# Performance work log

Measured on AMD Instinct MI355X. Metric: run time of the kernel, lower is better.

Reference implementation:

```python
import jax, jax.numpy as jnp
import numpy as np

NUM_SEG = 16384   # number of ranking lists (scope entries)
SEG_LEN = 512     # items per list
N = NUM_SEG * SEG_LEN


def setup_inputs() -> dict:
    key = jax.random.key(0)
    k1, k2, k3 = jax.random.split(key, 3)
    mean = jax.random.normal(k1, (N, 1), dtype=jnp.float32)
    variance = jax.random.uniform(k2, (N, 1), dtype=jnp.float32)
    targets = jax.random.normal(k3, (N,), dtype=jnp.float32)
    scope = jnp.full((NUM_SEG,), SEG_LEN, dtype=jnp.int32)  # segment lengths
    return {"mean": mean, "variance": variance, "scope": scope, "targets": targets}


def _seg_logsumexp(a, seg, num_segments):
    # numerically-stable segment-wise logsumexp (same math as log(sum(exp)))
    m = jax.ops.segment_max(a, seg, num_segments=num_segments)
    m = jnp.where(jnp.isfinite(m), m, jnp.zeros_like(m))
    s = jax.ops.segment_sum(jnp.exp(a - m[seg]), seg, num_segments=num_segments)
    return m + jnp.log(s)


def reference(mean, variance, scope, targets):
    num_segments = scope.shape[0]
    n = mean.shape[0]
    seg = jnp.repeat(jnp.arange(num_segments), scope, total_repeat_length=n)

    x = mean[:, 0]
    y = variance[:, 0]

    # Original per-segment math: pred_i = 1 / sum_j exp(x_j - x_i + (y_i + y_j)/2)
    #                           = exp(x_i - y_i/2) / sum_j exp(x_j + y_j/2)
    a = x + 0.5 * y
    logS = _seg_logsumexp(a, seg, num_segments)          # [num_segments]
    log_pred = x - 0.5 * y - logS[seg]                   # [N]

    # targ_i = 1 / sum_j exp(z_j - z_i) = softmax(z)_i within segment
    logZ = _seg_logsumexp(targets, seg, num_segments)
    targ = jnp.exp(targets - logZ[seg])                  # [N]

    # per-segment loss = -mean_i(targ_i * log pred_i)
    per_seg = -jax.ops.segment_sum(targ * log_pred, seg, num_segments=num_segments)
    per_seg = per_seg / scope.astype(mean.dtype)

    # losses summed over segments then divided by len(scope)
    return jnp.mean(per_seg).reshape(1)
```

## Files before the change

kernel.cpp:

```cpp
#include <hip/hip_runtime.h>
#include <hip/hip_bf16.h>
#include <math.h>

#define SEG_LEN 512
#define WAVES_PER_BLOCK 4

__device__ __forceinline__ float waveReduceSum(float v) {
    #pragma unroll
    for (int o = 32; o > 0; o >>= 1) v += __shfl_xor(v, o, 64);
    return v;
}

__global__ __launch_bounds__(256, 8) void listnet_seg_kernel(
    const float* __restrict__ mean,
    const float* __restrict__ variance,
    const int*   __restrict__ scope,
    const float* __restrict__ targets,
    float* __restrict__ per_seg_out,
    int num_seg)
{
    const int wave = threadIdx.x >> 6;
    const int lane = threadIdx.x & 63;
    const int seg  = blockIdx.x * WAVES_PER_BLOCK + wave;
    if (seg >= num_seg) return;

    const long long base = (long long)seg * SEG_LEN;
    const float4* m4 = (const float4*)(mean     + base);
    const float4* v4 = (const float4*)(variance + base);
    const float4* t4 = (const float4*)(targets  + base);

    float4 mx0 = m4[lane], mx1 = m4[lane + 64];
    float4 vy0 = v4[lane], vy1 = v4[lane + 64];
    float4 tt0 = t4[lane], tt1 = t4[lane + 64];

    float sA = 0.f, sT = 0.f, acc = 0.f;

    {
        float xs[8] = {mx0.x, mx0.y, mx0.z, mx0.w, mx1.x, mx1.y, mx1.z, mx1.w};
        float ys[8] = {vy0.x, vy0.y, vy0.z, vy0.w, vy1.x, vy1.y, vy1.z, vy1.w};
        float ts[8] = {tt0.x, tt0.y, tt0.z, tt0.w, tt1.x, tt1.y, tt1.z, tt1.w};
        #pragma unroll
        for (int i = 0; i < 8; ++i) {
            float a = fmaf(0.5f,  ys[i], xs[i]);
            float b = fmaf(-0.5f, ys[i], xs[i]);
            float et = __expf(ts[i]);
            sA += __expf(a);
            sT += et;
            acc = fmaf(et, b, acc);
        }
    }

    #pragma unroll
    for (int o = 32; o > 0; o >>= 1) {
        sA  += __shfl_xor(sA,  o, 64);
        sT  += __shfl_xor(sT,  o, 64);
        acc += __shfl_xor(acc, o, 64);
    }

    if (lane == 0) {
        float logS = __logf(sA);
        float per_seg = (logS * sT - acc) / (sT * (float)scope[seg]);
        per_seg_out[seg] = per_seg;
    }
}

__global__ __launch_bounds__(256) void listnet_finish_kernel(
    const float* __restrict__ per_seg, float* __restrict__ out, int num_seg)
{
    const float4* p4 = (const float4*)per_seg;
    const int n4 = num_seg >> 2;
    float s = 0.f;
    for (int i = threadIdx.x; i < n4; i += 256) {
        float4 v = p4[i];
        s += (v.x + v.y) + (v.z + v.w);
    }
    s = waveReduceSum(s);
    __shared__ float sm[WAVES_PER_BLOCK];
    const int wave = threadIdx.x >> 6;
    const int lane = threadIdx.x & 63;
    if (lane == 0) sm[wave] = s;
    __syncthreads();
    if (threadIdx.x == 0) {
        float tot = 0.f;
        #pragma unroll
        for (int w = 0; w < WAVES_PER_BLOCK; ++w) tot += sm[w];
        out[0] = tot / (float)num_seg;
    }
}

extern "C" void kernel_launch(void* const* d_in, const int* in_sizes, int n_in,
                              void* d_out, int out_size, void* d_ws, size_t ws_size,
                              hipStream_t stream) {
    const float* mean     = (const float*)d_in[0];
    const float* variance = (const float*)d_in[1];
    const int*   scope    = (const int*)d_in[2];
    const float* targets  = (const float*)d_in[3];
    float* out = (float*)d_out;

    const int num_seg = in_sizes[2];
    const int blocks = (num_seg + WAVES_PER_BLOCK - 1) / WAVES_PER_BLOCK;

    float* per_seg = (float*)d_ws;
    listnet_seg_kernel<<<blocks, 256, 0, stream>>>(
        mean, variance, scope, targets, per_seg, num_seg);
    listnet_finish_kernel<<<1, 256, 0, stream>>>(per_seg, out, num_seg);
}
```

Baseline: 121.7 us.

## Process two segments per wave and reduce per block before finish

```diff
diff --git a/kernel.cpp b/kernel.cpp
--- a/kernel.cpp
+++ b/kernel.cpp
@@ -3,7 +3,8 @@
 #include <math.h>
 
 #define SEG_LEN 512
-#define WAVES_PER_BLOCK 4
+#define WPB 4
+#define SPW 2
 
 __device__ __forceinline__ float waveReduceSum(float v) {
     #pragma unroll
@@ -11,71 +12,113 @@
     return v;
 }
 
-__global__ __launch_bounds__(256, 8) void listnet_seg_kernel(
+__device__ __forceinline__ float seg_result(float sA, float sT, float acc, float len) {
+    float logS = __logf(sA);
+    return (logS * sT - acc) / (sT * len);
+}
+
+__device__ __forceinline__ void accum8(const float4& m0, const float4& m1,
+                                       const float4& v0, const float4& v1,
+                                       const float4& t0, const float4& t1,
+                                       float& sA, float& sT, float& acc) {
+    float xs[8] = {m0.x, m0.y, m0.z, m0.w, m1.x, m1.y, m1.z, m1.w};
+    float ys[8] = {v0.x, v0.y, v0.z, v0.w, v1.x, v1.y, v1.z, v1.w};
+    float ts[8] = {t0.x, t0.y, t0.z, t0.w, t1.x, t1.y, t1.z, t1.w};
+    #pragma unroll
+    for (int i = 0; i < 8; ++i) {
+        float a = fmaf(0.5f,  ys[i], xs[i]);
+        float b = fmaf(-0.5f, ys[i], xs[i]);
+        float et = __expf(ts[i]);
+        sA += __expf(a);
+        sT += et;
+        acc = fmaf(et, b, acc);
+    }
+}
+
+__global__ __launch_bounds__(256) void listnet_seg_kernel(
     const float* __restrict__ mean,
     const float* __restrict__ variance,
     const int*   __restrict__ scope,
     const float* __restrict__ targets,
-    float* __restrict__ per_seg_out,
+    float* __restrict__ per_blk_out,
     int num_seg)
 {
     const int wave = threadIdx.x >> 6;
     const int lane = threadIdx.x & 63;
-    const int seg  = blockIdx.x * WAVES_PER_BLOCK + wave;
-    if (seg >= num_seg) return;
+    const int seg0 = (blockIdx.x * WPB + wave) * SPW;
 
-    const long long base = (long long)seg * SEG_LEN;
-    const float4* m4 = (const float4*)(mean     + base);
-    const float4* v4 = (const float4*)(variance + base);
-    const float4* t4 = (const float4*)(targets  + base);
+    float wave_part = 0.f;
 
-    float4 mx0 = m4[lane], mx1 = m4[lane + 64];
-    float4 vy0 = v4[lane], vy1 = v4[lane + 64];
-    float4 tt0 = t4[lane], tt1 = t4[lane + 64];
+    if (seg0 + 1 < num_seg) {
+        const long long base = (long long)seg0 * SEG_LEN;
+        const float4* m4 = (const float4*)(mean     + base);
+        const float4* v4 = (const float4*)(variance + base);
+        const float4* t4 = (const float4*)(targets  + base);
 
-    float sA = 0.f, sT = 0.f, acc = 0.f;
+        float4 mA0 = m4[lane],       mA1 = m4[lane + 64];
+        float4 vA0 = v4[lane],       vA1 = v4[lane + 64];
+        float4 tA0 = t4[lane],       tA1 = t4[lane + 64];
+        float4 mB0 = m4[lane + 128], mB1 = m4[lane + 192];
+        float4 vB0 = v4[lane + 128], vB1 = v4[lane + 192];
+        float4 tB0 = t4[lane + 128], tB1 = t4[lane + 192];
 
-    {
-        float xs[8] = {mx0.x, mx0.y, mx0.z, mx0.w, mx1.x, mx1.y, mx1.z, mx1.w};
-        float ys[8] = {vy0.x, vy0.y, vy0.z, vy0.w, vy1.x, vy1.y, vy1.z, vy1.w};
-        float ts[8] = {tt0.x, tt0.y, tt0.z, tt0.w, tt1.x, tt1.y, tt1.z, tt1.w};
+        float sA0 = 0.f, sT0 = 0.f, ac0 = 0.f;
+        float sA1 = 0.f, sT1 = 0.f, ac1 = 0.f;
+        accum8(mA0, mA1, vA0, vA1, tA0, tA1, sA0, sT0, ac0);
+        accum8(mB0, mB1, vB0, vB1, tB0, tB1, sA1, sT1, ac1);
+
         #pragma unroll
-        for (int i = 0; i < 8; ++i) {
-            float a = fmaf(0.5f,  ys[i], xs[i]);
-            float b = fmaf(-0.5f, ys[i], xs[i]);
-            float et = __expf(ts[i]);
-            sA += __expf(a);
-            sT += et;
-            acc = fmaf(et, b, acc);
+        for (int o = 32; o > 0; o >>= 1) {
+            sA0 += __shfl_xor(sA0, o, 64);
+            sT0 += __shfl_xor(sT0, o, 64);
+            ac0 += __shfl_xor(ac0, o, 64);
+            sA1 += __shfl_xor(sA1, o, 64);
+            sT1 += __shfl_xor(sT1, o, 64);
+            ac1 += __shfl_xor(ac1, o, 64);
+        }
+
+        if (lane == 0) {
+            wave_part = seg_result(sA0, sT0, ac0, (float)scope[seg0])
+                      + seg_result(sA1, sT1, ac1, (float)scope[seg0 + 1]);
+        }
+    } else if (seg0 < num_seg) {
+        for (int seg = seg0; seg < num_seg && seg < seg0 + SPW; ++seg) {
+            const long long base = (long long)seg * SEG_LEN;
+            const float4* m4 = (const float4*)(mean     + base);
+            const float4* v4 = (const float4*)(variance + base);
+            const float4* t4 = (const float4*)(targets  + base);
+            float4 m0 = m4[lane], m1 = m4[lane + 64];
+            float4 v0 = v4[lane], v1 = v4[lane + 64];
+            float4 t0 = t4[lane], t1 = t4[lane + 64];
+            float sA = 0.f, sT = 0.f, ac = 0.f;
+            accum8(m0, m1, v0, v1, t0, t1, sA, sT, ac);
+            sA = waveReduceSum(sA);
+            sT = waveReduceSum(sT);
+            ac = waveReduceSum(ac);
+            if (lane == 0)
+                wave_part += seg_result(sA, sT, ac, (float)scope[seg]);
         }
     }
 
-    #pragma unroll
-    for (int o = 32; o > 0; o >>= 1) {
-        sA  += __shfl_xor(sA,  o, 64);
-        sT  += __shfl_xor(sT,  o, 64);
-        acc += __shfl_xor(acc, o, 64);
-    }
-
-    if (lane == 0) {
-        float logS = __logf(sA);
-        float per_seg = (logS * sT - acc) / (sT * (float)scope[seg]);
-        per_seg_out[seg] = per_seg;
+    __shared__ float sm[WPB];
+    if (lane == 0) sm[wave] = wave_part;
+    __syncthreads();
+    if (threadIdx.x == 0) {
+        float t = 0.f;
+        #pragma unroll
+        for (int w = 0; w < WPB; ++w) t += sm[w];
+        per_blk_out[blockIdx.x] = t;
     }
 }
 
 __global__ __launch_bounds__(256) void listnet_finish_kernel(
-    const float* __restrict__ per_seg, float* __restrict__ out, int num_seg)
+    const float* __restrict__ per_blk, float* __restrict__ out,
+    int n_blk, int num_seg)
 {
-    const float4* p4 = (const float4*)per_seg;
-    const int n4 = num_seg >> 2;
     float s = 0.f;
-    for (int i = threadIdx.x; i < n4; i += 256) {
-        float4 v = p4[i];
-        s += (v.x + v.y) + (v.z + v.w);
-    }
+    for (int i = threadIdx.x; i < n_blk; i += 256) s += per_blk[i];
     s = waveReduceSum(s);
-    __shared__ float sm[WAVES_PER_BLOCK];
+    __shared__ float sm[WPB];
     const int wave = threadIdx.x >> 6;
     const int lane = threadIdx.x & 63;
     if (lane == 0) sm[wave] = s;
@@ -83,7 +126,7 @@
     if (threadIdx.x == 0) {
         float tot = 0.f;
         #pragma unroll
-        for (int w = 0; w < WAVES_PER_BLOCK; ++w) tot += sm[w];
+        for (int w = 0; w < WPB; ++w) tot += sm[w];
         out[0] = tot / (float)num_seg;
     }
 }
@@ -98,10 +141,11 @@
     float* out = (float*)d_out;
 
     const int num_seg = in_sizes[2];
-    const int blocks = (num_seg + WAVES_PER_BLOCK - 1) / WAVES_PER_BLOCK;
+    const int segs_per_block = WPB * SPW;
+    const int blocks = (num_seg + segs_per_block - 1) / segs_per_block;
 
-    float* per_seg = (float*)d_ws;
+    float* per_blk = (float*)d_ws;
     listnet_seg_kernel<<<blocks, 256, 0, stream>>>(
-        mean, variance, scope, targets, per_seg, num_seg);
-    listnet_finish_kernel<<<1, 256, 0, stream>>>(per_seg, out, num_seg);
+        mean, variance, scope, targets, per_blk, num_seg);
+    listnet_finish_kernel<<<1, 256, 0, stream>>>(per_blk, out, blocks, num_seg);
 }
```

After: 120.1 us. About the same (-1.3%).
